# Kernel tuning notes

Measured on AMD Instinct MI355X. Metric: run time of the kernel, lower is better.

The kernel has to match this reference:

```python
import jax, jax.numpy as jnp
import numpy as np

DIM = 256
H = 4
HD = DIM // H
SCALE = HD ** -0.5
W = 10
PAD = W // 2
MAX_LEN = 512


def setup_inputs() -> dict:
    key = jax.random.key(0)
    ks = jax.random.split(key, 32)
    B, T, D = 32, 512, DIM
    def w(k, shape):
        return jax.random.normal(k, shape, dtype=jnp.float32) * 0.02
    inp = {
        'x': jax.random.normal(ks[0], (B, T, D), dtype=jnp.float32),
        # global TemporalAttention params (weights stored as (in,out))
        'gq_w': w(ks[1], (D, D)), 'gq_b': jnp.zeros((D,), jnp.float32),
        'gk_w': w(ks[2], (D, D)), 'gk_b': jnp.zeros((D,), jnp.float32),
        'gv_w': w(ks[3], (D, D)), 'gv_b': jnp.zeros((D,), jnp.float32),
        'go_w': w(ks[4], (D, D)), 'go_b': jnp.zeros((D,), jnp.float32),
        'rel_pos_bias': w(ks[5], (2 * MAX_LEN - 1, H)),
        # local sliding-window attention params
        'lq_w': w(ks[6], (D, D)), 'lq_b': jnp.zeros((D,), jnp.float32),
        'lk_w': w(ks[7], (D, D)), 'lk_b': jnp.zeros((D,), jnp.float32),
        'lv_w': w(ks[8], (D, D)), 'lv_b': jnp.zeros((D,), jnp.float32),
        # pattern attention (only q/k projections matter for returned weights)
        'pattern_embed': jax.random.normal(ks[9], (1, 3, D), dtype=jnp.float32),
        'pq_w': w(ks[10], (D, D)), 'pq_b': jnp.zeros((D,), jnp.float32),
        'pk_w': w(ks[11], (D, D)), 'pk_b': jnp.zeros((D,), jnp.float32),
        # fusion MLP
        'f1_w': w(ks[12], (2 * D, D)), 'f1_b': jnp.zeros((D,), jnp.float32),
        'f2_w': w(ks[13], (D, D)), 'f2_b': jnp.zeros((D,), jnp.float32),
    }
    return inp


def _forward(x, gq_w, gq_b, gk_w, gk_b, gv_w, gv_b, go_w, go_b, rel_pos_bias,
             lq_w, lq_b, lk_w, lk_b, lv_w, lv_b,
             pattern_embed, pq_w, pq_b, pk_w, pk_b,
             f1_w, f1_b, f2_w, f2_b):
    B, T, D = x.shape
    # ---- global temporal attention ----
    q = (x @ gq_w + gq_b).reshape(B, T, H, HD)
    k = (x @ gk_w + gk_b).reshape(B, T, H, HD)
    v = (x @ gv_w + gv_b).reshape(B, T, H, HD)
    attn = jnp.einsum('bthd,bshd->bhts', q, k) * SCALE  # (B,H,T,T)
    pos = jnp.arange(T)
    idx = jnp.clip(pos[None, :] - pos[:, None] + T - 1, 0, 2 * T - 2)  # (T,T)
    attn = attn + jnp.transpose(rel_pos_bias[idx], (2, 0, 1))[None]
    attn_w = jax.nn.softmax(attn, axis=-1)  # dropout = identity in eval
    g_out = jnp.einsum('bhts,bshd->bthd', attn_w, v).reshape(B, T, D)
    global_out = g_out @ go_w + go_b
    # ---- local sliding-window attention (single head over full dim) ----
    x_pad = jnp.pad(x, ((0, 0), (PAD, PAD), (0, 0)))  # zero pad -> k/v get bias
    lq = x @ lq_w + lq_b                      # (B,T,D)
    lk = x_pad @ lk_w + lk_b                  # (B,T+W,D)
    lv = x_pad @ lv_w + lv_b
    widx = jnp.arange(T)[:, None] + jnp.arange(W)[None, :]  # (T,W)
    k_win = lk[:, widx]                       # (B,T,W,D)
    v_win = lv[:, widx]
    l_attn = jax.nn.softmax(jnp.einsum('btd,btwd->btw', lq, k_win) * SCALE, axis=-1)
    local_out = jnp.einsum('btw,btwd->btd', l_attn, v_win)
    # ---- fusion MLP + residual ----
    fused = jnp.concatenate([global_out, local_out], axis=-1)
    output = jax.nn.relu(fused @ f1_w + f1_b) @ f2_w + f2_b + x
    # ---- pattern attention (torch MHA, weights averaged over heads) ----
    pe = jnp.broadcast_to(pattern_embed, (B, 3, D))
    pooled = jnp.mean(x, axis=1, keepdims=True)  # (B,1,D)
    pq = (pooled @ pq_w + pq_b).reshape(B, 1, H, HD)
    pk = (pe @ pk_w + pk_b).reshape(B, 3, H, HD)
    plogits = jnp.einsum('bqhd,bkhd->bhqk', pq, pk) * SCALE  # (B,H,1,3)
    pw = jax.nn.softmax(plogits, axis=-1).mean(axis=1)  # avg over heads -> (B,1,3)
    pattern_scores = pw[:, 0]  # (B,3)
    return output, pattern_scores


def reference(x, gq_w, gq_b, gk_w, gk_b, gv_w, gv_b, go_w, go_b, rel_pos_bias,
              lq_w, lq_b, lk_w, lk_b, lv_w, lv_b,
              pattern_embed, pq_w, pq_b, pk_w, pk_b,
              f1_w, f1_b, f2_w, f2_b):
    return _forward(x, gq_w, gq_b, gk_w, gk_b, gv_w, gv_b, go_w, go_b, rel_pos_bias,
                    lq_w, lq_b, lk_w, lk_b, lv_w, lv_b,
                    pattern_embed, pq_w, pq_b, pk_w, pk_b,
                    f1_w, f1_b, f2_w, f2_b)
```

## Files before the change

kernel.cpp:

```cpp
#include <hip/hip_runtime.h>
#include <hip/hip_bf16.h>

typedef __attribute__((ext_vector_type(8))) __bf16 bf16x8;
typedef __attribute__((ext_vector_type(8))) unsigned short u16x8;
typedef __attribute__((ext_vector_type(4))) float f32x4;

#define MFMA_BF16(a,b,c) __builtin_amdgcn_mfma_f32_16x16x32_bf16((a),(b),(c),0,0,0)

#define ASCALE 0.125f
#define SEQT 512
#define NB 32
#define BT 16384

#define GLD_LDS16(g, l) __builtin_amdgcn_global_load_lds( \
    (__attribute__((address_space(1))) void*)(g), \
    (__attribute__((address_space(3))) void*)(l), 16, 0, 0)

__device__ __forceinline__ unsigned short f2bf(float f) {
    unsigned int u = __float_as_uint(f);
    u += 0x7fffu + ((u >> 16) & 1u);
    return (unsigned short)(u >> 16);
}
__device__ __forceinline__ float bf2f(unsigned short h) {
    return __uint_as_float(((unsigned int)h) << 16);
}

__global__ __launch_bounds__(256) void cast_x_kernel(const float* __restrict__ x,
                                                     unsigned short* __restrict__ xb, int n) {
    int i = (blockIdx.x * 256 + threadIdx.x) * 4;
    if (i < n) {
        float4 v = *(const float4*)(x + i);
        ushort4 o;
        o.x = f2bf(v.x); o.y = f2bf(v.y); o.z = f2bf(v.z); o.w = f2bf(v.w);
        *(ushort4*)(xb + i) = o;
    }
}

struct WPack {
    const float* src[9];
    unsigned short* dst[9];
    int K[9];
    const float* bsrc[5];
    float* bdst;
};

__global__ __launch_bounds__(256) void wconv_all(WPack p) {
    const int z = blockIdx.z;
    const int tid = threadIdx.x;
    if (z == 9) {
        int idx = blockIdx.y * 8 + blockIdx.x;
        if (idx < 5) p.bdst[idx * 256 + tid] = p.bsrc[idx][tid];
        return;
    }
    const int K = p.K[z];
    const int k0 = blockIdx.x * 64;
    if (k0 >= K) return;
    const int n0 = blockIdx.y * 64;
    __shared__ float tile[64][65];
    const int tx = tid & 63, ty = tid >> 6;
    const float* src = p.src[z];
    #pragma unroll
    for (int i = 0; i < 16; ++i) {
        int r = ty * 16 + i;
        tile[r][tx] = src[(size_t)(k0 + r) * 256 + n0 + tx];
    }
    __syncthreads();
    unsigned short* dst = p.dst[z];
    #pragma unroll
    for (int i = 0; i < 16; ++i) {
        int r = ty * 16 + i;
        dst[(size_t)(n0 + r) * K + k0 + tx] = f2bf(tile[tx][r]);
    }
}

template<int BN>
__global__ __launch_bounds__(256)
void gemm_db(const unsigned short* __restrict__ A, const unsigned short* __restrict__ Bt,
             const float* __restrict__ bias, int K,
             void* __restrict__ out, int ldc, int mode, int do_relu, int bias_row,
             const float* __restrict__ resid) {
    constexpr int BM = 128;
    constexpr int MF = (BN == 128) ? 4 : 2;
    constexpr int AR = (BM * 32) / 2048;
    constexpr int BR = (BN * 32) / 2048;
    __shared__ __align__(16) unsigned short As[2][BM * 32];
    __shared__ __align__(16) unsigned short Bs[2][BN * 32];
    const int tid = threadIdx.x;
    const int w = tid >> 6, l = tid & 63, g = l >> 4, rl = l & 15;
    const int wrow = (BN == 128) ? (w >> 1) * 64 : w * 32;
    const int wcol = (BN == 128) ? (w & 1) * 64 : 0;
    const int m0 = blockIdx.x * BM, n0 = blockIdx.y * BN;

    f32x4 acc[MF][4];
    #pragma unroll
    for (int m = 0; m < MF; ++m)
        #pragma unroll
        for (int n = 0; n < 4; ++n) acc[m][n] = (f32x4){0.f, 0.f, 0.f, 0.f};

    auto stage = [&](int buf, int k0) {
        #pragma unroll
        for (int j = 0; j < AR; ++j) {
            int e = j * 256 + tid;
            GLD_LDS16(A + (size_t)(m0 + (e >> 2)) * K + k0 + (e & 3) * 8, &As[buf][e * 8]);
        }
        #pragma unroll
        for (int j = 0; j < BR; ++j) {
            int e = j * 256 + tid;
            GLD_LDS16(Bt + (size_t)(n0 + (e >> 2)) * K + k0 + (e & 3) * 8, &Bs[buf][e * 8]);
        }
    };

    const int NIT = K >> 5;
    stage(0, 0);
    __syncthreads();
    for (int it = 0; it < NIT; ++it) {
        const int cur = it & 1;
        if (it + 1 < NIT) stage(cur ^ 1, (it + 1) * 32);
        bf16x8 af[MF], bfr[4];
        #pragma unroll
        for (int m = 0; m < MF; ++m)
            af[m] = *(const bf16x8*)&As[cur][(wrow + m * 16 + rl) * 32 + g * 8];
        #pragma unroll
        for (int n = 0; n < 4; ++n)
            bfr[n] = *(const bf16x8*)&Bs[cur][(wcol + n * 16 + rl) * 32 + g * 8];
        #pragma unroll
        for (int m = 0; m < MF; ++m)
            #pragma unroll
            for (int n = 0; n < 4; ++n)
                acc[m][n] = MFMA_BF16(af[m], bfr[n], acc[m][n]);
        __syncthreads();
    }

    #pragma unroll
    for (int m = 0; m < MF; ++m) {
        #pragma unroll
        for (int n = 0; n < 4; ++n) {
            #pragma unroll
            for (int r = 0; r < 4; ++r) {
                int row = m0 + wrow + m * 16 + g * 4 + r;
                int col = n0 + wcol + n * 16 + rl;
                float v = acc[m][n][r] + (bias_row ? bias[row] : bias[col]);
                if (do_relu) v = fmaxf(v, 0.f);
                if (mode == 0) {
                    ((unsigned short*)out)[(size_t)row * ldc + col] = f2bf(v);
                } else {
                    float res = resid ? resid[(size_t)row * ldc + col] : 0.f;
                    ((float*)out)[(size_t)row * ldc + col] = v + res;
                }
            }
        }
    }
}

__global__ __launch_bounds__(256)
void attn_global2(const unsigned short* __restrict__ proj, const unsigned short* __restrict__ vT,
                  const float* __restrict__ rpb, unsigned short* __restrict__ gout) {
    __shared__ __align__(16) unsigned short Ks[64][72];
    __shared__ __align__(16) unsigned short Vs[64][72];
    __shared__ __align__(16) unsigned short Ps[64][72];
    __shared__ float rb_s[127];

    const int tid = threadIdx.x;
    const int w = tid >> 6, l = tid & 63, g = l >> 4, rl = l & 15;
    const int bh = blockIdx.y, b = bh >> 2, h = bh & 3;
    const int t0 = blockIdx.x * 64;

    bf16x8 qf[2];
    #pragma unroll
    for (int kk = 0; kk < 2; ++kk)
        qf[kk] = *(const bf16x8*)(proj + (size_t)(b * SEQT + t0 + w * 16 + rl) * 1280
                                  + h * 64 + kk * 32 + g * 8);

    f32x4 oacc[4];
    #pragma unroll
    for (int n = 0; n < 4; ++n) oacc[n] = (f32x4){0.f, 0.f, 0.f, 0.f};
    float lpart[4] = {0.f, 0.f, 0.f, 0.f};

    for (int s0 = 0; s0 < SEQT; s0 += 64) {
        __syncthreads();
        #pragma unroll
        for (int cc = 0; cc < 2; ++cc) {
            int c = tid + cc * 256;
            int sr = c >> 3, hc = c & 7;
            u16x8 kv = *(const u16x8*)(proj + (size_t)(b * SEQT + s0 + sr) * 1280
                                       + 256 + h * 64 + hc * 8);
            *(u16x8*)&Ks[sr][hc * 8] = kv;
            u16x8 vv = *(const u16x8*)(vT + (size_t)(h * 64 + sr) * BT
                                       + b * SEQT + s0 + hc * 8);
            *(u16x8*)&Vs[sr][hc * 8] = vv;
        }
        if (tid < 127) {
            int dd = s0 - t0 + 448 + tid;
            rb_s[tid] = rpb[dd * 4 + h];
        }
        __syncthreads();

        f32x4 sacc[4];
        #pragma unroll
        for (int n = 0; n < 4; ++n) sacc[n] = (f32x4){0.f, 0.f, 0.f, 0.f};
        #pragma unroll
        for (int kk = 0; kk < 2; ++kk) {
            #pragma unroll
            for (int n = 0; n < 4; ++n) {
                bf16x8 kf = *(const bf16x8*)&Ks[n * 16 + rl][kk * 32 + g * 8];
                sacc[n] = MFMA_BF16(qf[kk], kf, sacc[n]);
            }
        }

        #pragma unroll
        for (int n = 0; n < 4; ++n) {
            #pragma unroll
            for (int r = 0; r < 4; ++r) {
                int relc = (n * 16 + rl) - (w * 16 + g * 4 + r) + 63;
                float p = __expf(sacc[n][r] * ASCALE + rb_s[relc]);
                lpart[r] += p;
                Ps[w * 16 + g * 4 + r][n * 16 + rl] = f2bf(p);
            }
        }

        #pragma unroll
        for (int kk = 0; kk < 2; ++kk) {
            bf16x8 pf = *(const bf16x8*)&Ps[w * 16 + rl][kk * 32 + g * 8];
            #pragma unroll
            for (int n = 0; n < 4; ++n) {
                bf16x8 vf = *(const bf16x8*)&Vs[n * 16 + rl][kk * 32 + g * 8];
                oacc[n] = MFMA_BF16(pf, vf, oacc[n]);
            }
        }
    }

    #pragma unroll
    for (int r = 0; r < 4; ++r) {
        #pragma unroll
        for (int mk = 1; mk < 16; mk <<= 1) lpart[r] += __shfl_xor(lpart[r], mk);
    }
    const size_t obase = (size_t)b * SEQT * 256 + h * 64;
    #pragma unroll
    for (int n = 0; n < 4; ++n) {
        #pragma unroll
        for (int r = 0; r < 4; ++r) {
            float o = oacc[n][r] / lpart[r];
            gout[obase + (size_t)(t0 + w * 16 + g * 4 + r) * 256 + n * 16 + rl] = f2bf(o);
        }
    }
}

__global__ __launch_bounds__(256)
void local_attn(const unsigned short* __restrict__ proj,
                const float* __restrict__ lk_bias, const float* __restrict__ lv_bias,
                unsigned short* __restrict__ fused) {
    const int tid = threadIdx.x;
    const int wv = tid >> 6, lane = tid & 63;
    const int row = blockIdx.x * 4 + wv;
    const int b = row >> 9, tt = row & 511;

    ushort4 qv = *((const ushort4*)(proj + (size_t)row * 1280 + 512) + lane);
    float qf[4] = {bf2f(qv.x), bf2f(qv.y), bf2f(qv.z), bf2f(qv.w)};

    float sw[10];
    #pragma unroll
    for (int w = 0; w < 10; ++w) {
        int src = tt + w - 5;
        float kf[4];
        if (src >= 0 && src < 512) {
            ushort4 kv = *((const ushort4*)(proj + (size_t)(b * 512 + src) * 1280 + 768) + lane);
            kf[0] = bf2f(kv.x); kf[1] = bf2f(kv.y); kf[2] = bf2f(kv.z); kf[3] = bf2f(kv.w);
        } else {
            float4 kb4 = *((const float4*)lk_bias + lane);
            kf[0] = kb4.x; kf[1] = kb4.y; kf[2] = kb4.z; kf[3] = kb4.w;
        }
        float p = qf[0] * kf[0] + qf[1] * kf[1] + qf[2] * kf[2] + qf[3] * kf[3];
        #pragma unroll
        for (int mk = 1; mk < 64; mk <<= 1) p += __shfl_xor(p, mk);
        sw[w] = p * ASCALE;
    }
    float mx = sw[0];
    #pragma unroll
    for (int w = 1; w < 10; ++w) mx = fmaxf(mx, sw[w]);
    float pv[10], s = 0.f;
    #pragma unroll
    for (int w = 0; w < 10; ++w) { pv[w] = __expf(sw[w] - mx); s += pv[w]; }
    float inv = 1.f / s;

    float of[4] = {0.f, 0.f, 0.f, 0.f};
    #pragma unroll
    for (int w = 0; w < 10; ++w) {
        int src = tt + w - 5;
        float vf[4];
        if (src >= 0 && src < 512) {
            ushort4 vv = *((const ushort4*)(proj + (size_t)(b * 512 + src) * 1280 + 1024) + lane);
            vf[0] = bf2f(vv.x); vf[1] = bf2f(vv.y); vf[2] = bf2f(vv.z); vf[3] = bf2f(vv.w);
        } else {
            float4 vb4 = *((const float4*)lv_bias + lane);
            vf[0] = vb4.x; vf[1] = vb4.y; vf[2] = vb4.z; vf[3] = vb4.w;
        }
        float pw = pv[w] * inv;
        of[0] += pw * vf[0]; of[1] += pw * vf[1]; of[2] += pw * vf[2]; of[3] += pw * vf[3];
    }
    ushort4 o;
    o.x = f2bf(of[0]); o.y = f2bf(of[1]); o.z = f2bf(of[2]); o.w = f2bf(of[3]);
    *((ushort4*)(fused + (size_t)row * 512 + 256) + lane) = o;
}

__global__ __launch_bounds__(256)
void pooled_part(const unsigned short* __restrict__ xb, float* __restrict__ pp) {
    int b = blockIdx.x >> 3, tc = blockIdx.x & 7;
    int d = threadIdx.x;
    const unsigned short* xp = xb + ((size_t)b * SEQT + tc * 64) * 256 + d;
    float s = 0.f;
    #pragma unroll 8
    for (int t = 0; t < 64; ++t) s += bf2f(xp[(size_t)t * 256]);
    pp[(size_t)(tc * 32 + b) * 256 + d] = s * (1.0f / 512.0f);
}

__global__ __launch_bounds__(256)
void pattern_k(const float* __restrict__ pp, const float* __restrict__ pe,
               const float* __restrict__ pq_w, const float* __restrict__ pq_b,
               const float* __restrict__ pk_w, const float* __restrict__ pk_b,
               float* __restrict__ out_scores) {
    __shared__ float pool_s[256];
    __shared__ float pes[3 * 256];
    __shared__ float pq_s[256];
    __shared__ float pk_s[3][256];
    __shared__ float pw_s[4][3];
    int b = blockIdx.x, d = threadIdx.x;
    float ps = 0.f;
    #pragma unroll
    for (int tc = 0; tc < 8; ++tc) ps += pp[(size_t)(tc * 32 + b) * 256 + d];
    pool_s[d] = ps;
    pes[d] = pe[d]; pes[256 + d] = pe[256 + d]; pes[512 + d] = pe[512 + d];
    __syncthreads();
    float acc = pq_b[d];
    for (int k = 0; k < 256; ++k) acc += pool_s[k] * pq_w[k * 256 + d];
    pq_s[d] = acc;
    for (int j = 0; j < 3; ++j) {
        float a = pk_b[d];
        for (int k = 0; k < 256; ++k) a += pes[j * 256 + k] * pk_w[k * 256 + d];
        pk_s[j][d] = a;
    }
    __syncthreads();
    int h = d >> 6, lane = d & 63;
    float lg[3];
    #pragma unroll
    for (int j = 0; j < 3; ++j) {
        float p = pq_s[h * 64 + lane] * pk_s[j][h * 64 + lane];
        #pragma unroll
        for (int mk = 1; mk < 64; mk <<= 1) p += __shfl_xor(p, mk);
        lg[j] = p * ASCALE;
    }
    float mx = fmaxf(fmaxf(lg[0], lg[1]), lg[2]);
    float e0 = __expf(lg[0] - mx), e1 = __expf(lg[1] - mx), e2 = __expf(lg[2] - mx);
    float sinv = 1.f / (e0 + e1 + e2);
    if (lane == 0) { pw_s[h][0] = e0 * sinv; pw_s[h][1] = e1 * sinv; pw_s[h][2] = e2 * sinv; }
    __syncthreads();
    if (d < 3)
        out_scores[b * 3 + d] = 0.25f * (pw_s[0][d] + pw_s[1][d] + pw_s[2][d] + pw_s[3][d]);
}

extern "C" void kernel_launch(void* const* d_in, const int* in_sizes, int n_in,
                              void* d_out, int out_size, void* d_ws, size_t ws_size,
                              hipStream_t stream) {
    (void)in_sizes; (void)n_in; (void)out_size; (void)ws_size;
    const float* x    = (const float*)d_in[0];
    const float* gq_w = (const float*)d_in[1];  const float* gq_b = (const float*)d_in[2];
    const float* gk_w = (const float*)d_in[3];  const float* gk_b = (const float*)d_in[4];
    const float* gv_w = (const float*)d_in[5];  const float* gv_b = (const float*)d_in[6];
    const float* go_w = (const float*)d_in[7];  const float* go_b = (const float*)d_in[8];
    const float* rpb  = (const float*)d_in[9];
    const float* lq_w = (const float*)d_in[10]; const float* lq_b = (const float*)d_in[11];
    const float* lk_w = (const float*)d_in[12]; const float* lk_b = (const float*)d_in[13];
    const float* lv_w = (const float*)d_in[14]; const float* lv_b = (const float*)d_in[15];
    const float* pe   = (const float*)d_in[16];
    const float* pq_w = (const float*)d_in[17]; const float* pq_b = (const float*)d_in[18];
    const float* pk_w = (const float*)d_in[19]; const float* pk_b = (const float*)d_in[20];
    const float* f1_w = (const float*)d_in[21]; const float* f1_b = (const float*)d_in[22];
    const float* f2_w = (const float*)d_in[23]; const float* f2_b = (const float*)d_in[24];

    char* ws = (char*)d_ws;
    const size_t MB = 1024 * 1024;
    unsigned short* xb    = (unsigned short*)(ws + 0);
    unsigned short* proj  = (unsigned short*)(ws + 8 * MB);
    unsigned short* vT    = (unsigned short*)(ws + 48 * MB);
    unsigned short* fused = (unsigned short*)(ws + 56 * MB);
    unsigned short* hb    = (unsigned short*)(ws + 72 * MB);
    unsigned short* wts   = (unsigned short*)(ws + 80 * MB);
    unsigned short* gv_t  = wts;
    unsigned short* go_t  = gv_t + 65536;
    unsigned short* f1_t  = go_t + 65536;
    unsigned short* f2_t  = f1_t + 131072;
    unsigned short* wcat  = f2_t + 65536;
    float* bcat = (float*)(ws + 82 * MB);
    float* pp   = (float*)(ws + 83 * MB);

    float* out = (float*)d_out;
    float* out_scores = out + (size_t)BT * 256;

    cast_x_kernel<<<4096, 256, 0, stream>>>(x, xb, BT * 256);
    WPack p;
    p.src[0] = gq_w; p.dst[0] = wcat + 0 * 65536; p.K[0] = 256;
    p.src[1] = gk_w; p.dst[1] = wcat + 1 * 65536; p.K[1] = 256;
    p.src[2] = lq_w; p.dst[2] = wcat + 2 * 65536; p.K[2] = 256;
    p.src[3] = lk_w; p.dst[3] = wcat + 3 * 65536; p.K[3] = 256;
    p.src[4] = lv_w; p.dst[4] = wcat + 4 * 65536; p.K[4] = 256;
    p.src[5] = gv_w; p.dst[5] = gv_t;  p.K[5] = 256;
    p.src[6] = go_w; p.dst[6] = go_t;  p.K[6] = 256;
    p.src[7] = f1_w; p.dst[7] = f1_t;  p.K[7] = 512;
    p.src[8] = f2_w; p.dst[8] = f2_t;  p.K[8] = 256;
    p.bsrc[0] = gq_b; p.bsrc[1] = gk_b; p.bsrc[2] = lq_b; p.bsrc[3] = lk_b; p.bsrc[4] = lv_b;
    p.bdst = bcat;
    wconv_all<<<dim3(8, 4, 10), 256, 0, stream>>>(p);
    pooled_part<<<256, 256, 0, stream>>>(xb, pp);

    gemm_db<128><<<dim3(BT / 128, 10), 256, 0, stream>>>(xb, wcat, bcat, 256, proj, 1280, 0, 0, 0, nullptr);
    gemm_db<64><<<dim3(2, BT / 64), 256, 0, stream>>>(gv_t, xb, gv_b, 256, vT, BT, 0, 0, 1, nullptr);

    attn_global2<<<dim3(SEQT / 64, NB * 4), 256, 0, stream>>>(proj, vT, rpb, xb);

    gemm_db<64><<<dim3(BT / 128, 4), 256, 0, stream>>>(xb, go_t, go_b, 256, fused, 512, 0, 0, 0, nullptr);

    local_attn<<<BT / 4, 256, 0, stream>>>(proj, lk_b, lv_b, fused);

    gemm_db<64><<<dim3(BT / 128, 4), 256, 0, stream>>>(fused, f1_t, f1_b, 512, hb, 256, 0, 1, 0, nullptr);
    gemm_db<64><<<dim3(BT / 128, 4), 256, 0, stream>>>(hb, f2_t, f2_b, 256, out, 256, 1, 0, 0, x);

    pattern_k<<<NB, 256, 0, stream>>>(pp, pe, pq_w, pq_b, pk_w, pk_b, out_scores);
}
```

Before: 299.7 us.

## Rewrite bf16 GEMM with 64-wide K tiles, XOR-swizzled LDS, and finer waitcnt sync

Replaces the double-buffered GEMM with a version that stages 64 K-elements per iteration instead of 32, halving the loop trip count and barrier count. It adds an XOR swizzle on LDS chunk placement so MFMA fragment loads avoid bank conflicts. It also swaps __syncthreads for an explicit vmcnt wait plus s_barrier, so the prefetch of the next tile can stay in flight. Tile shapes for the smaller GEMMs change to 64x128 with a new warp layout. The cost is twice the LDS footprint per block, which can reduce occupancy.

```diff
diff --git a/kernel.cpp b/kernel.cpp
--- a/kernel.cpp
+++ b/kernel.cpp
@@ -73,68 +73,82 @@
     }
 }
 
-template<int BN>
+template<int BM, int BN>
 __global__ __launch_bounds__(256)
-void gemm_db(const unsigned short* __restrict__ A, const unsigned short* __restrict__ Bt,
+void gemm_v3(const unsigned short* __restrict__ A, const unsigned short* __restrict__ Bt,
              const float* __restrict__ bias, int K,
              void* __restrict__ out, int ldc, int mode, int do_relu, int bias_row,
              const float* __restrict__ resid) {
-    constexpr int BM = 128;
-    constexpr int MF = (BN == 128) ? 4 : 2;
-    constexpr int AR = (BM * 32) / 2048;
-    constexpr int BR = (BN * 32) / 2048;
-    __shared__ __align__(16) unsigned short As[2][BM * 32];
-    __shared__ __align__(16) unsigned short Bs[2][BN * 32];
+    constexpr int CA = BM / 32;
+    constexpr int CB = BN / 32;
+    constexpr int MFM = 4;
+    constexpr int MFN = (BM == 128) ? 4 : 2;
+    __shared__ __align__(16) unsigned short As[2][BM * 64];
+    __shared__ __align__(16) unsigned short Bs[2][BN * 64];
     const int tid = threadIdx.x;
     const int w = tid >> 6, l = tid & 63, g = l >> 4, rl = l & 15;
-    const int wrow = (BN == 128) ? (w >> 1) * 64 : w * 32;
-    const int wcol = (BN == 128) ? (w & 1) * 64 : 0;
+    const int wrow = (BM == 128) ? (w >> 1) * 64 : 0;
+    const int wcol = (BM == 128) ? (w & 1) * 64 : w * 32;
     const int m0 = blockIdx.x * BM, n0 = blockIdx.y * BN;
 
-    f32x4 acc[MF][4];
-    #pragma unroll
-    for (int m = 0; m < MF; ++m)
-        #pragma unroll
-        for (int n = 0; n < 4; ++n) acc[m][n] = (f32x4){0.f, 0.f, 0.f, 0.f};
+    f32x4 acc[MFM][MFN];
+    #pragma unroll
+    for (int m = 0; m < MFM; ++m)
+        #pragma unroll
+        for (int n = 0; n < MFN; ++n) acc[m][n] = (f32x4){0.f, 0.f, 0.f, 0.f};
 
     auto stage = [&](int buf, int k0) {
         #pragma unroll
-        for (int j = 0; j < AR; ++j) {
+        for (int j = 0; j < CA; ++j) {
             int e = j * 256 + tid;
-            GLD_LDS16(A + (size_t)(m0 + (e >> 2)) * K + k0 + (e & 3) * 8, &As[buf][e * 8]);
-        }
-        #pragma unroll
-        for (int j = 0; j < BR; ++j) {
+            int r = e >> 3, sp = e & 7;
+            int kc = (sp ^ (r & 7)) * 8;
+            GLD_LDS16(A + (size_t)(m0 + r) * K + k0 + kc, &As[buf][e * 8]);
+        }
+        #pragma unroll
+        for (int j = 0; j < CB; ++j) {
             int e = j * 256 + tid;
-            GLD_LDS16(Bt + (size_t)(n0 + (e >> 2)) * K + k0 + (e & 3) * 8, &Bs[buf][e * 8]);
+            int r = e >> 3, sp = e & 7;
+            int kc = (sp ^ (r & 7)) * 8;
+            GLD_LDS16(Bt + (size_t)(n0 + r) * K + k0 + kc, &Bs[buf][e * 8]);
         }
     };
 
-    const int NIT = K >> 5;
+    const int NIT = K >> 6;
     stage(0, 0);
-    __syncthreads();
+    const int sx = (rl & 7);
     for (int it = 0; it < NIT; ++it) {
         const int cur = it & 1;
-        if (it + 1 < NIT) stage(cur ^ 1, (it + 1) * 32);
-        bf16x8 af[MF], bfr[4];
-        #pragma unroll
-        for (int m = 0; m < MF; ++m)
-            af[m] = *(const bf16x8*)&As[cur][(wrow + m * 16 + rl) * 32 + g * 8];
-        #pragma unroll
-        for (int n = 0; n < 4; ++n)
-            bfr[n] = *(const bf16x8*)&Bs[cur][(wcol + n * 16 + rl) * 32 + g * 8];
-        #pragma unroll
-        for (int m = 0; m < MF; ++m)
-            #pragma unroll
-            for (int n = 0; n < 4; ++n)
-                acc[m][n] = MFMA_BF16(af[m], bfr[n], acc[m][n]);
-        __syncthreads();
-    }
-
-    #pragma unroll
-    for (int m = 0; m < MF; ++m) {
-        #pragma unroll
-        for (int n = 0; n < 4; ++n) {
+        if (it + 1 < NIT) {
+            stage(cur ^ 1, (it + 1) << 6);
+            asm volatile("s_waitcnt vmcnt(%0)" :: "n"(CA + CB) : "memory");
+        } else {
+            asm volatile("s_waitcnt vmcnt(0)" ::: "memory");
+        }
+        __builtin_amdgcn_s_barrier();
+        #pragma unroll
+        for (int kk = 0; kk < 2; ++kk) {
+            const int co = ((kk * 4 + g) ^ sx) * 8;
+            bf16x8 af[MFM], bf_[MFN];
+            #pragma unroll
+            for (int m = 0; m < MFM; ++m)
+                af[m] = *(const bf16x8*)&As[cur][(wrow + m * 16 + rl) * 64 + co];
+            #pragma unroll
+            for (int n = 0; n < MFN; ++n)
+                bf_[n] = *(const bf16x8*)&Bs[cur][(wcol + n * 16 + rl) * 64 + co];
+            #pragma unroll
+            for (int m = 0; m < MFM; ++m)
+                #pragma unroll
+                for (int n = 0; n < MFN; ++n)
+                    acc[m][n] = MFMA_BF16(af[m], bf_[n], acc[m][n]);
+        }
+        __builtin_amdgcn_s_barrier();
+    }
+
+    #pragma unroll
+    for (int m = 0; m < MFM; ++m) {
+        #pragma unroll
+        for (int n = 0; n < MFN; ++n) {
             #pragma unroll
             for (int r = 0; r < 4; ++r) {
                 int row = m0 + wrow + m * 16 + g * 4 + r;
@@ -411,17 +425,17 @@
     wconv_all<<<dim3(8, 4, 10), 256, 0, stream>>>(p);
     pooled_part<<<256, 256, 0, stream>>>(xb, pp);
 
-    gemm_db<128><<<dim3(BT / 128, 10), 256, 0, stream>>>(xb, wcat, bcat, 256, proj, 1280, 0, 0, 0, nullptr);
-    gemm_db<64><<<dim3(2, BT / 64), 256, 0, stream>>>(gv_t, xb, gv_b, 256, vT, BT, 0, 0, 1, nullptr);
+    gemm_v3<128, 128><<<dim3(BT / 128, 10), 256, 0, stream>>>(xb, wcat, bcat, 256, proj, 1280, 0, 0, 0, nullptr);
+    gemm_v3<64, 128><<<dim3(4, BT / 128), 256, 0, stream>>>(gv_t, xb, gv_b, 256, vT, BT, 0, 0, 1, nullptr);
 
     attn_global2<<<dim3(SEQT / 64, NB * 4), 256, 0, stream>>>(proj, vT, rpb, xb);
 
-    gemm_db<64><<<dim3(BT / 128, 4), 256, 0, stream>>>(xb, go_t, go_b, 256, fused, 512, 0, 0, 0, nullptr);
+    gemm_v3<64, 128><<<dim3(BT / 64, 2), 256, 0, stream>>>(xb, go_t, go_b, 256, fused, 512, 0, 0, 0, nullptr);
 
     local_attn<<<BT / 4, 256, 0, stream>>>(proj, lk_b, lv_b, fused);
 
-    gemm_db<64><<<dim3(BT / 128, 4), 256, 0, stream>>>(fused, f1_t, f1_b, 512, hb, 256, 0, 1, 0, nullptr);
-    gemm_db<64><<<dim3(BT / 128, 4), 256, 0, stream>>>(hb, f2_t, f2_b, 256, out, 256, 1, 0, 0, x);
+    gemm_v3<64, 128><<<dim3(BT / 64, 2), 256, 0, stream>>>(fused, f1_t, f1_b, 512, hb, 256, 0, 1, 0, nullptr);
+    gemm_v3<64, 128><<<dim3(BT / 64, 2), 256, 0, stream>>>(hb, f2_t, f2_b, 256, out, 256, 1, 0, 0, x);
 
     pattern_k<<<NB, 256, 0, stream>>>(pp, pe, pq_w, pq_b, pk_w, pk_b, out_scores);
 }
```

After: 306.2 us. 2.2% more time.

## Replace LDS double-buffered GEMM with per-wave direct-global-load GEMM

Applied to the files above, without the earlier changes.

Replaces the shared-memory double-buffered GEMM, which staged tiles through LDS with global_load_lds and block barriers, with a kernel where each wave loads its MFMA fragments straight from global memory into registers and computes an independent 64x64 output tile. This removes LDS traffic and __syncthreads from the inner loop. In exchange, operands are no longer shared across the waves of a block, which raises global and L2 traffic, and load latency can only be hidden through the unroll by 2 and occupancy. Launch grids are reshaped to match the new per-wave tiling.

```diff
diff --git a/kernel.cpp b/kernel.cpp
--- a/kernel.cpp
+++ b/kernel.cpp
@@ -11,10 +11,6 @@
 #define SEQT 512
 #define NB 32
 #define BT 16384
-
-#define GLD_LDS16(g, l) __builtin_amdgcn_global_load_lds( \
-    (__attribute__((address_space(1))) void*)(g), \
-    (__attribute__((address_space(3))) void*)(l), 16, 0, 0)
 
 __device__ __forceinline__ unsigned short f2bf(float f) {
     unsigned int u = __float_as_uint(f);
@@ -73,72 +69,50 @@
     }
 }
 
-template<int BN>
 __global__ __launch_bounds__(256)
-void gemm_db(const unsigned short* __restrict__ A, const unsigned short* __restrict__ Bt,
-             const float* __restrict__ bias, int K,
-             void* __restrict__ out, int ldc, int mode, int do_relu, int bias_row,
-             const float* __restrict__ resid) {
-    constexpr int BM = 128;
-    constexpr int MF = (BN == 128) ? 4 : 2;
-    constexpr int AR = (BM * 32) / 2048;
-    constexpr int BR = (BN * 32) / 2048;
-    __shared__ __align__(16) unsigned short As[2][BM * 32];
-    __shared__ __align__(16) unsigned short Bs[2][BN * 32];
+void gemm_w(const unsigned short* __restrict__ A, const unsigned short* __restrict__ Bt,
+            const float* __restrict__ bias, int K,
+            void* __restrict__ out, int ldc, int mode, int do_relu, int bias_row,
+            const float* __restrict__ resid) {
     const int tid = threadIdx.x;
     const int w = tid >> 6, l = tid & 63, g = l >> 4, rl = l & 15;
-    const int wrow = (BN == 128) ? (w >> 1) * 64 : w * 32;
-    const int wcol = (BN == 128) ? (w & 1) * 64 : 0;
-    const int m0 = blockIdx.x * BM, n0 = blockIdx.y * BN;
-
-    f32x4 acc[MF][4];
-    #pragma unroll
-    for (int m = 0; m < MF; ++m)
+    const int mb = (blockIdx.x * 4 + w) * 64;
+    const int nb = blockIdx.y * 64;
+
+    f32x4 acc[4][4];
+    #pragma unroll
+    for (int m = 0; m < 4; ++m)
         #pragma unroll
         for (int n = 0; n < 4; ++n) acc[m][n] = (f32x4){0.f, 0.f, 0.f, 0.f};
 
-    auto stage = [&](int buf, int k0) {
-        #pragma unroll
-        for (int j = 0; j < AR; ++j) {
-            int e = j * 256 + tid;
-            GLD_LDS16(A + (size_t)(m0 + (e >> 2)) * K + k0 + (e & 3) * 8, &As[buf][e * 8]);
-        }
-        #pragma unroll
-        for (int j = 0; j < BR; ++j) {
-            int e = j * 256 + tid;
-            GLD_LDS16(Bt + (size_t)(n0 + (e >> 2)) * K + k0 + (e & 3) * 8, &Bs[buf][e * 8]);
-        }
-    };
-
-    const int NIT = K >> 5;
-    stage(0, 0);
-    __syncthreads();
-    for (int it = 0; it < NIT; ++it) {
-        const int cur = it & 1;
-        if (it + 1 < NIT) stage(cur ^ 1, (it + 1) * 32);
-        bf16x8 af[MF], bfr[4];
-        #pragma unroll
-        for (int m = 0; m < MF; ++m)
-            af[m] = *(const bf16x8*)&As[cur][(wrow + m * 16 + rl) * 32 + g * 8];
-        #pragma unroll
-        for (int n = 0; n < 4; ++n)
-            bfr[n] = *(const bf16x8*)&Bs[cur][(wcol + n * 16 + rl) * 32 + g * 8];
-        #pragma unroll
-        for (int m = 0; m < MF; ++m)
+    const unsigned short* ap = A  + (size_t)(mb + rl) * K + g * 8;
+    const unsigned short* bp = Bt + (size_t)(nb + rl) * K + g * 8;
+    const size_t rstep = (size_t)16 * K;
+
+    const int NKK = K >> 5;
+    #pragma unroll 2
+    for (int kk = 0; kk < NKK; ++kk) {
+        const int ko = kk * 32;
+        bf16x8 af[4], bf_[4];
+        #pragma unroll
+        for (int m = 0; m < 4; ++m) af[m]  = *(const bf16x8*)(ap + m * rstep + ko);
+        #pragma unroll
+        for (int n = 0; n < 4; ++n) bf_[n] = *(const bf16x8*)(bp + n * rstep + ko);
+        #pragma unroll
+        for (int m = 0; m < 4; ++m)
             #pragma unroll
             for (int n = 0; n < 4; ++n)
-                acc[m][n] = MFMA_BF16(af[m], bfr[n], acc[m][n]);
-        __syncthreads();
-    }
-
-    #pragma unroll
-    for (int m = 0; m < MF; ++m) {
+                acc[m][n] = MFMA_BF16(af[m], bf_[n], acc[m][n]);
+    }
+
+    #pragma unroll
+    for (int m = 0; m < 4; ++m) {
         #pragma unroll
         for (int n = 0; n < 4; ++n) {
             #pragma unroll
             for (int r = 0; r < 4; ++r) {
-                int row = m0 + wrow + m * 16 + g * 4 + r;
-                int col = n0 + wcol + n * 16 + rl;
+                int row = mb + m * 16 + g * 4 + r;
+                int col = nb + n * 16 + rl;
                 float v = acc[m][n][r] + (bias_row ? bias[row] : bias[col]);
                 if (do_relu) v = fmaxf(v, 0.f);
                 if (mode == 0) {
@@ -411,17 +385,17 @@
     wconv_all<<<dim3(8, 4, 10), 256, 0, stream>>>(p);
     pooled_part<<<256, 256, 0, stream>>>(xb, pp);
 
-    gemm_db<128><<<dim3(BT / 128, 10), 256, 0, stream>>>(xb, wcat, bcat, 256, proj, 1280, 0, 0, 0, nullptr);
-    gemm_db<64><<<dim3(2, BT / 64), 256, 0, stream>>>(gv_t, xb, gv_b, 256, vT, BT, 0, 0, 1, nullptr);
+    gemm_w<<<dim3(BT / 256, 20), 256, 0, stream>>>(xb, wcat, bcat, 256, proj, 1280, 0, 0, 0, nullptr);
+    gemm_w<<<dim3(1, BT / 64), 256, 0, stream>>>(gv_t, xb, gv_b, 256, vT, BT, 0, 0, 1, nullptr);
 
     attn_global2<<<dim3(SEQT / 64, NB * 4), 256, 0, stream>>>(proj, vT, rpb, xb);
 
-    gemm_db<64><<<dim3(BT / 128, 4), 256, 0, stream>>>(xb, go_t, go_b, 256, fused, 512, 0, 0, 0, nullptr);
+    gemm_w<<<dim3(BT / 256, 4), 256, 0, stream>>>(xb, go_t, go_b, 256, fused, 512, 0, 0, 0, nullptr);
 
     local_attn<<<BT / 4, 256, 0, stream>>>(proj, lk_b, lv_b, fused);
 
-    gemm_db<64><<<dim3(BT / 128, 4), 256, 0, stream>>>(fused, f1_t, f1_b, 512, hb, 256, 0, 1, 0, nullptr);
-    gemm_db<64><<<dim3(BT / 128, 4), 256, 0, stream>>>(hb, f2_t, f2_b, 256, out, 256, 1, 0, 0, x);
+    gemm_w<<<dim3(BT / 256, 4), 256, 0, stream>>>(fused, f1_t, f1_b, 512, hb, 256, 0, 1, 0, nullptr);
+    gemm_w<<<dim3(BT / 256, 4), 256, 0, stream>>>(hb, f2_t, f2_b, 256, out, 256, 1, 0, 0, x);
 
     pattern_k<<<NB, 256, 0, stream>>>(pp, pe, pq_w, pq_b, pk_w, pk_b, out_scores);
 }
```

New measurement: 363.0 us. 21.1% more time.
